# Kernel tuning notes

Measured on AMD Instinct MI355X. Metric: run time of the kernel, lower is better.

The kernel has to match this reference:

```python
import jax, jax.numpy as jnp
import numpy as np

N = 50000
E = 800000
D = 128
L = 2


def setup_inputs() -> dict:
    key = jax.random.key(0)
    ks = jax.random.split(key, 8)
    x = jax.random.normal(ks[0], (N, D), dtype=jnp.float32)
    edge_index = jax.random.randint(ks[1], (2, E), 0, N, dtype=jnp.int64)
    s = 1.0 / np.sqrt(D)
    Wl = jax.random.uniform(ks[2], (L, D, D), jnp.float32, -s, s)  # neighbor transform (with bias)
    bl = jax.random.uniform(ks[3], (L, D), jnp.float32, -s, s)
    Wr = jax.random.uniform(ks[4], (L, D, D), jnp.float32, -s, s)  # root/self transform (no bias)
    W = jax.random.uniform(ks[5], (D, D), jnp.float32, -s, s)      # final Linear
    b = jax.random.uniform(ks[6], (D,), jnp.float32, -s, s)
    return {"x": x, "edge_index": edge_index, "Wl": Wl, "bl": bl, "Wr": Wr, "W": W, "b": b}


def reference(x, edge_index, Wl, bl, Wr, W, b):
    src, dst = edge_index[0], edge_index[1]
    n = x.shape[0]
    for l in range(Wl.shape[0]):
        # gather neighbor (source) features, scatter-max into destination nodes
        agg = jax.ops.segment_max(x[src], dst, num_segments=n)  # [N, D]
        agg = jnp.where(jnp.isneginf(agg), 0.0, agg)  # PyG: isolated nodes -> 0
        # SAGEConv: lin_l(agg) + lin_r(x)
        x = agg @ Wl[l].T + bl[l] + x @ Wr[l].T
        x = jax.nn.relu(x)
    return x @ W.T + b
```

## Files before the change

kernel.cpp:

```cpp
#include <hip/hip_runtime.h>
#include <math.h>

#define NN 50000
#define NE 800000
#define DD 128
#define NBUCK 196
#define PTILE 4096
#define PBLOCKS 196
#define CONVB 6250

typedef unsigned short u16;
typedef short s8v __attribute__((ext_vector_type(8)));
typedef float f16v __attribute__((ext_vector_type(16)));

__device__ __forceinline__ u16 f2bf(float f) {
    unsigned u = __float_as_uint(f);
    return (u16)((u + 0x7FFFu + ((u >> 16) & 1u)) >> 16);
}
__device__ __forceinline__ float bflo(unsigned u) { return __uint_as_float(u << 16); }
__device__ __forceinline__ float bfhi(unsigned u) { return __uint_as_float(u & 0xFFFF0000u); }

__device__ __forceinline__ void pack_one(const float* __restrict__ Wl,
                                         const float* __restrict__ Wr,
                                         bool two, int o, u16* __restrict__ out) {
    int j = o & 7;
    int l = (o >> 3) & 63;
    int cn = o >> 9;
    int n = cn & 3;
    int c = cn >> 2;
    int colj = n * 32 + (l & 31);
    int k = c * 16 + (l >> 5) * 8 + j;
    float v;
    if (two) v = (k < DD) ? Wl[colj * DD + k] : Wr[colj * DD + (k - DD)];
    else     v = Wl[colj * DD + k];
    out[o] = f2bf(v);
}

__global__ __launch_bounds__(256) void prep_kernel(
        const float4* __restrict__ x4, ushort4* __restrict__ hb0,
        const float* __restrict__ Wl, const float* __restrict__ Wr,
        const float* __restrict__ W,
        u16* __restrict__ Bpk0, u16* __restrict__ Bpk1, u16* __restrict__ Bpkf,
        int* __restrict__ bcnt) {
    int bid = blockIdx.x;
    int tid = threadIdx.x;
    if (bid < CONVB) {
        int i = bid * 256 + tid;
        float4 v = x4[i];
        ushort4 o;
        o.x = f2bf(v.x); o.y = f2bf(v.y); o.z = f2bf(v.z); o.w = f2bf(v.w);
        hb0[i] = o;
    } else if (bid < CONVB + 128) {
        pack_one(Wl, Wr, true, (bid - CONVB) * 256 + tid, Bpk0);
    } else if (bid < CONVB + 256) {
        pack_one(Wl + DD * DD, Wr + DD * DD, true, (bid - CONVB - 128) * 256 + tid, Bpk1);
    } else if (bid < CONVB + 320) {
        pack_one(W, W, false, (bid - CONVB - 256) * 256 + tid, Bpkf);
    } else {
        if (tid < NBUCK) bcnt[tid] = 0;
    }
}

__global__ __launch_bounds__(256) void bucket_hist(const int* __restrict__ ei,
                                                   int* __restrict__ bcnt) {
    __shared__ int h[NBUCK];
    for (int i = threadIdx.x; i < NBUCK; i += 256) h[i] = 0;
    __syncthreads();
    int e0 = blockIdx.x * PTILE;
#pragma unroll
    for (int i = 0; i < 16; i++) {
        int e = e0 + i * 256 + threadIdx.x;
        if (e < NE) atomicAdd(&h[ei[NE + e] >> 8], 1);
    }
    __syncthreads();
    for (int i = threadIdx.x; i < NBUCK; i += 256)
        if (h[i]) atomicAdd(&bcnt[i], h[i]);
}

__global__ __launch_bounds__(256) void bucket_scan(const int* __restrict__ bcnt,
                                                   int* __restrict__ bbase,
                                                   int* __restrict__ bcur,
                                                   int* __restrict__ rowptr) {
    __shared__ int s[256];
    int t = threadIdx.x;
    int v = (t < NBUCK) ? bcnt[t] : 0;
    s[t] = v;
    __syncthreads();
    for (int o = 1; o < 256; o <<= 1) {
        int u = (t >= o) ? s[t - o] : 0;
        __syncthreads();
        s[t] += u;
        __syncthreads();
    }
    int ex = s[t] - v;
    if (t < NBUCK) { bbase[t] = ex; bcur[t] = ex; }
    if (t == 0) rowptr[NN] = NE;
}

__global__ __launch_bounds__(256) void bucket_partition(const int* __restrict__ ei,
                                                        int* __restrict__ bcur,
                                                        unsigned* __restrict__ packed) {
    __shared__ int h[NBUCK];
    __shared__ int base[NBUCK];
    int t = threadIdx.x;
    for (int i = t; i < NBUCK; i += 256) h[i] = 0;
    __syncthreads();
    int e0 = blockIdx.x * PTILE;
    int dsts[16], srcs[16];
#pragma unroll
    for (int i = 0; i < 16; i++) {
        int e = e0 + i * 256 + t;
        if (e < NE) {
            dsts[i] = ei[NE + e];
            srcs[i] = ei[e];
            atomicAdd(&h[dsts[i] >> 8], 1);
        } else dsts[i] = -1;
    }
    __syncthreads();
    for (int i = t; i < NBUCK; i += 256) {
        int c = h[i];
        base[i] = c ? atomicAdd(&bcur[i], c) : 0;
    }
    __syncthreads();
    for (int i = t; i < NBUCK; i += 256) h[i] = 0;
    __syncthreads();
#pragma unroll
    for (int i = 0; i < 16; i++) {
        if (dsts[i] >= 0) {
            int bk = dsts[i] >> 8;
            int r = atomicAdd(&h[bk], 1);
            packed[base[bk] + r] = (unsigned)srcs[i] | ((unsigned)(dsts[i] & 255) << 16);
        }
    }
}

__global__ __launch_bounds__(256) void bucket_csr(const unsigned* __restrict__ packed,
                                                  const int* __restrict__ bcnt,
                                                  const int* __restrict__ bbase,
                                                  int* __restrict__ rowptr,
                                                  int* __restrict__ col) {
    __shared__ int deg[256];
    __shared__ int off[256];
    int bk = blockIdx.x;
    int cnt = bcnt[bk], base = bbase[bk];
    int t = threadIdx.x;
    deg[t] = 0;
    __syncthreads();
    for (int i = t; i < cnt; i += 256) atomicAdd(&deg[packed[base + i] >> 16], 1);
    __syncthreads();
    int v = deg[t];
    off[t] = v;
    __syncthreads();
    for (int o = 1; o < 256; o <<= 1) {
        int u = (t >= o) ? off[t - o] : 0;
        __syncthreads();
        off[t] += u;
        __syncthreads();
    }
    int ex = off[t] - v;
    int node = (bk << 8) + t;
    if (node < NN) rowptr[node] = base + ex;
    deg[t] = ex;
    __syncthreads();
    for (int i = t; i < cnt; i += 256) {
        unsigned p = packed[base + i];
        int dl = p >> 16;
        int r = atomicAdd(&deg[dl], 1);
        col[base + r] = (int)(p & 0xFFFFu);
    }
}

__device__ __forceinline__ void vmax8(float* m, uint4 v) {
    m[0] = fmaxf(m[0], bflo(v.x)); m[1] = fmaxf(m[1], bfhi(v.x));
    m[2] = fmaxf(m[2], bflo(v.y)); m[3] = fmaxf(m[3], bfhi(v.y));
    m[4] = fmaxf(m[4], bflo(v.z)); m[5] = fmaxf(m[5], bfhi(v.z));
    m[6] = fmaxf(m[6], bflo(v.w)); m[7] = fmaxf(m[7], bfhi(v.w));
}

template<bool FINAL>
__global__ __launch_bounds__(256) void fused_layer(
        const u16* __restrict__ hsrc,
        const int* __restrict__ rowptr,
        const int* __restrict__ col,
        const u16* __restrict__ Bpk,
        const float* __restrict__ bias,
        const u16* __restrict__ Bpkf,
        const float* __restrict__ bfin,
        void* __restrict__ outv) {
    __shared__ u16 As[128 * 128];
    char* Ab = (char*)As;
    int tid = threadIdx.x;
    int row0 = blockIdx.x * 128;
    const uint4* xb4 = (const uint4*)hsrc;

    {
        int j = tid & 15;
        int nl0 = tid >> 4;
        for (int p = 0; p < 8; p++) {
            int rl = (p << 4) + nl0;
            int node = row0 + rl;
            uint4 o = make_uint4(0u, 0u, 0u, 0u);
            if (node < NN) {
                int s0 = rowptr[node], s1 = rowptr[node + 1];
                if (s0 < s1) {
                    float m0[8], m1[8], m2[8], m3[8];
#pragma unroll
                    for (int q = 0; q < 8; q++) { m0[q] = m1[q] = m2[q] = m3[q] = -INFINITY; }
                    int i = s0;
                    for (; i + 8 <= s1; i += 8) {
                        int c0 = col[i],     c1 = col[i + 1], c2 = col[i + 2], c3 = col[i + 3];
                        int c4 = col[i + 4], c5 = col[i + 5], c6 = col[i + 6], c7 = col[i + 7];
                        uint4 v0 = xb4[(size_t)c0 * 16 + j];
                        uint4 v1 = xb4[(size_t)c1 * 16 + j];
                        uint4 v2 = xb4[(size_t)c2 * 16 + j];
                        uint4 v3 = xb4[(size_t)c3 * 16 + j];
                        uint4 v4 = xb4[(size_t)c4 * 16 + j];
                        uint4 v5 = xb4[(size_t)c5 * 16 + j];
                        uint4 v6 = xb4[(size_t)c6 * 16 + j];
                        uint4 v7 = xb4[(size_t)c7 * 16 + j];
                        vmax8(m0, v0); vmax8(m1, v1); vmax8(m2, v2); vmax8(m3, v3);
                        vmax8(m0, v4); vmax8(m1, v5); vmax8(m2, v6); vmax8(m3, v7);
                    }
                    for (; i + 4 <= s1; i += 4) {
                        int c0 = col[i], c1 = col[i + 1], c2 = col[i + 2], c3 = col[i + 3];
                        uint4 v0 = xb4[(size_t)c0 * 16 + j];
                        uint4 v1 = xb4[(size_t)c1 * 16 + j];
                        uint4 v2 = xb4[(size_t)c2 * 16 + j];
                        uint4 v3 = xb4[(size_t)c3 * 16 + j];
                        vmax8(m0, v0); vmax8(m1, v1); vmax8(m2, v2); vmax8(m3, v3);
                    }
                    for (; i < s1; i++) {
                        uint4 v = xb4[(size_t)col[i] * 16 + j];
                        vmax8(m0, v);
                    }
#pragma unroll
                    for (int q = 0; q < 8; q++)
                        m0[q] = fmaxf(fmaxf(m0[q], m1[q]), fmaxf(m2[q], m3[q]));
                    o.x = (__float_as_uint(m0[0]) >> 16) | (__float_as_uint(m0[1]) & 0xFFFF0000u);
                    o.y = (__float_as_uint(m0[2]) >> 16) | (__float_as_uint(m0[3]) & 0xFFFF0000u);
                    o.z = (__float_as_uint(m0[4]) >> 16) | (__float_as_uint(m0[5]) & 0xFFFF0000u);
                    o.w = (__float_as_uint(m0[6]) >> 16) | (__float_as_uint(m0[7]) & 0xFFFF0000u);
                }
            }
            *(uint4*)(Ab + rl * 256 + ((j << 4) ^ ((rl & 7) << 4))) = o;
        }
    }
    __syncthreads();

    int wt = tid >> 6;
    int lane = tid & 63;
    int arl = wt * 32 + (lane & 31);
    int rg = row0 + arl;
    if (rg > NN - 1) rg = NN - 1;
    int koff = (lane >> 5) * 8;
    int swz = (arl & 7) << 4;
    const s8v* Bv = (const s8v*)Bpk;

    f16v acc[4];
#pragma unroll
    for (int n = 0; n < 4; n++) acc[n] = (f16v)(0.0f);

#pragma unroll
    for (int c = 0; c < 16; c++) {
        s8v a;
        if (c < 8)
            a = *(const s8v*)(Ab + arl * 256 + (((c * 16 + koff) * 2) ^ swz));
        else
            a = *(const s8v*)(hsrc + (size_t)rg * DD + (c - 8) * 16 + koff);
#pragma unroll
        for (int n = 0; n < 4; n++) {
            s8v b = Bv[(c * 4 + n) * 64 + lane];
            acc[n] = __builtin_amdgcn_mfma_f32_32x32x16_bf16(a, b, acc[n], 0, 0, 0);
        }
    }

    int rowadd = 4 * (lane >> 5);
    if constexpr (!FINAL) {
        u16* hdst = (u16*)outv;
#pragma unroll
        for (int n = 0; n < 4; n++) {
            int colj = n * 32 + (lane & 31);
            float bj = bias[colj];
#pragma unroll
            for (int r = 0; r < 16; r++) {
                int row = row0 + wt * 32 + (r & 3) + 8 * (r >> 2) + rowadd;
                if (row < NN)
                    hdst[(size_t)row * DD + colj] = f2bf(fmaxf(acc[n][r] + bj, 0.0f));
            }
        }
    } else {
        __syncthreads();
#pragma unroll
        for (int n = 0; n < 4; n++) {
            int colj = n * 32 + (lane & 31);
            float bj = bias[colj];
#pragma unroll
            for (int r = 0; r < 16; r++) {
                int rloc = wt * 32 + (r & 3) + 8 * (r >> 2) + rowadd;
                float v = fmaxf(acc[n][r] + bj, 0.0f);
                *(u16*)(Ab + rloc * 256 + ((colj * 2) ^ ((rloc & 7) << 4))) = f2bf(v);
            }
        }
        __syncthreads();
        const s8v* Bvf = (const s8v*)Bpkf;
        f16v acc2[4];
#pragma unroll
        for (int n = 0; n < 4; n++) acc2[n] = (f16v)(0.0f);
#pragma unroll
        for (int c = 0; c < 8; c++) {
            s8v a = *(const s8v*)(Ab + arl * 256 + (((c * 16 + koff) * 2) ^ swz));
#pragma unroll
            for (int n = 0; n < 4; n++) {
                s8v b = Bvf[(c * 4 + n) * 64 + lane];
                acc2[n] = __builtin_amdgcn_mfma_f32_32x32x16_bf16(a, b, acc2[n], 0, 0, 0);
            }
        }
        float* fout = (float*)outv;
#pragma unroll
        for (int n = 0; n < 4; n++) {
            int colj = n * 32 + (lane & 31);
            float bj = bfin[colj];
#pragma unroll
            for (int r = 0; r < 16; r++) {
                int row = row0 + wt * 32 + (r & 3) + 8 * (r >> 2) + rowadd;
                if (row < NN)
                    fout[(size_t)row * DD + colj] = acc2[n][r] + bj;
            }
        }
    }
}

extern "C" void kernel_launch(void* const* d_in, const int* in_sizes, int n_in,
                              void* d_out, int out_size, void* d_ws, size_t ws_size,
                              hipStream_t stream) {
    const float* x  = (const float*)d_in[0];
    const int*   ei = (const int*)d_in[1];
    const float* Wl = (const float*)d_in[2];
    const float* bl = (const float*)d_in[3];
    const float* Wr = (const float*)d_in[4];
    const float* W  = (const float*)d_in[5];
    const float* b  = (const float*)d_in[6];
    float* out = (float*)d_out;

    u16* aggb = (u16*)d_ws;
    u16* hb0  = aggb + (size_t)NN * DD;
    u16* hb1  = hb0 + (size_t)NN * DD;
    u16* Bpk0 = hb1 + (size_t)NN * DD;
    u16* Bpk1 = Bpk0 + 32768;
    u16* Bpkf = Bpk1 + 32768;
    unsigned* packed = (unsigned*)(Bpkf + 16384);
    int* col    = (int*)(packed + NE);
    int* rowptr = col + NE;
    int* bcnt   = rowptr + NN + 1;
    int* bbase  = bcnt + NBUCK;
    int* bcur   = bbase + NBUCK;

    dim3 blk(256);
    int gemmBlocks = (NN + 127) / 128;
    int prepBlocks = CONVB + 320 + 1;

    prep_kernel<<<prepBlocks, blk, 0, stream>>>(
        (const float4*)x, (ushort4*)hb0, Wl, Wr, W, Bpk0, Bpk1, Bpkf, bcnt);

    bucket_hist<<<PBLOCKS, blk, 0, stream>>>(ei, bcnt);
    bucket_scan<<<1, blk, 0, stream>>>(bcnt, bbase, bcur, rowptr);
    bucket_partition<<<PBLOCKS, blk, 0, stream>>>(ei, bcur, packed);
    bucket_csr<<<NBUCK, blk, 0, stream>>>(packed, bcnt, bbase, rowptr, col);

    fused_layer<false><<<gemmBlocks, blk, 0, stream>>>(
        hb0, rowptr, col, Bpk0, bl, nullptr, nullptr, hb1);

    fused_layer<true><<<gemmBlocks, blk, 0, stream>>>(
        hb1, rowptr, col, Bpk1, bl + DD, Bpkf, b, out);
}
```

Measured before the change: 247.8 us.

## Split fused aggregate+GEMM into separate kernels and fold CSR build steps

```diff
diff --git a/kernel.cpp b/kernel.cpp
--- a/kernel.cpp
+++ b/kernel.cpp
@@ -5,8 +5,8 @@
 #define NE 800000
 #define DD 128
 #define NBUCK 196
-#define PTILE 4096
-#define PBLOCKS 196
+#define EPB 2048
+#define PB 391
 #define CONVB 6250
 
 typedef unsigned short u16;
@@ -19,6 +19,11 @@
 }
 __device__ __forceinline__ float bflo(unsigned u) { return __uint_as_float(u << 16); }
 __device__ __forceinline__ float bfhi(unsigned u) { return __uint_as_float(u & 0xFFFF0000u); }
+
+__global__ __launch_bounds__(256) void zero_kernel(int* __restrict__ p, int n) {
+    int i = threadIdx.x + blockIdx.x * 256;
+    if (i < n) p[i] = 0;
+}
 
 __device__ __forceinline__ void pack_one(const float* __restrict__ Wl,
                                          const float* __restrict__ Wr,
@@ -41,7 +46,7 @@
         const float* __restrict__ Wl, const float* __restrict__ Wr,
         const float* __restrict__ W,
         u16* __restrict__ Bpk0, u16* __restrict__ Bpk1, u16* __restrict__ Bpkf,
-        int* __restrict__ bcnt) {
+        const int* __restrict__ ei, int* __restrict__ bcnt) {
     int bid = blockIdx.x;
     int tid = threadIdx.x;
     if (bid < CONVB) {
@@ -57,58 +62,48 @@
     } else if (bid < CONVB + 320) {
         pack_one(W, W, false, (bid - CONVB - 256) * 256 + tid, Bpkf);
     } else {
-        if (tid < NBUCK) bcnt[tid] = 0;
-    }
-}
-
-__global__ __launch_bounds__(256) void bucket_hist(const int* __restrict__ ei,
-                                                   int* __restrict__ bcnt) {
-    __shared__ int h[NBUCK];
-    for (int i = threadIdx.x; i < NBUCK; i += 256) h[i] = 0;
-    __syncthreads();
-    int e0 = blockIdx.x * PTILE;
-#pragma unroll
-    for (int i = 0; i < 16; i++) {
-        int e = e0 + i * 256 + threadIdx.x;
-        if (e < NE) atomicAdd(&h[ei[NE + e] >> 8], 1);
-    }
-    __syncthreads();
-    for (int i = threadIdx.x; i < NBUCK; i += 256)
-        if (h[i]) atomicAdd(&bcnt[i], h[i]);
-}
-
-__global__ __launch_bounds__(256) void bucket_scan(const int* __restrict__ bcnt,
-                                                   int* __restrict__ bbase,
-                                                   int* __restrict__ bcur,
-                                                   int* __restrict__ rowptr) {
-    __shared__ int s[256];
-    int t = threadIdx.x;
-    int v = (t < NBUCK) ? bcnt[t] : 0;
-    s[t] = v;
-    __syncthreads();
-    for (int o = 1; o < 256; o <<= 1) {
-        int u = (t >= o) ? s[t - o] : 0;
-        __syncthreads();
-        s[t] += u;
-        __syncthreads();
-    }
-    int ex = s[t] - v;
-    if (t < NBUCK) { bbase[t] = ex; bcur[t] = ex; }
-    if (t == 0) rowptr[NN] = NE;
+        __shared__ int h[NBUCK];
+        for (int i = tid; i < NBUCK; i += 256) h[i] = 0;
+        __syncthreads();
+        int e0 = (bid - (CONVB + 320)) * EPB;
+#pragma unroll
+        for (int i = 0; i < 8; i++) {
+            int e = e0 + i * 256 + tid;
+            if (e < NE) atomicAdd(&h[ei[NE + e] >> 8], 1);
+        }
+        __syncthreads();
+        for (int i = tid; i < NBUCK; i += 256)
+            if (h[i]) atomicAdd(&bcnt[i], h[i]);
+    }
 }
 
 __global__ __launch_bounds__(256) void bucket_partition(const int* __restrict__ ei,
-                                                        int* __restrict__ bcur,
-                                                        unsigned* __restrict__ packed) {
+                                                        const int* __restrict__ bcnt,
+                                                        int* __restrict__ claim,
+                                                        unsigned* __restrict__ packed,
+                                                        int* __restrict__ rowptr) {
+    __shared__ int sc[256];
+    __shared__ int bb[NBUCK];
     __shared__ int h[NBUCK];
     __shared__ int base[NBUCK];
     int t = threadIdx.x;
+    int v = (t < NBUCK) ? bcnt[t] : 0;
+    sc[t] = v;
+    __syncthreads();
+    for (int o = 1; o < 256; o <<= 1) {
+        int u = (t >= o) ? sc[t - o] : 0;
+        __syncthreads();
+        sc[t] += u;
+        __syncthreads();
+    }
+    if (t < NBUCK) bb[t] = sc[t] - v;
+    if (t == 0 && blockIdx.x == 0) rowptr[NN] = NE;
     for (int i = t; i < NBUCK; i += 256) h[i] = 0;
     __syncthreads();
-    int e0 = blockIdx.x * PTILE;
-    int dsts[16], srcs[16];
-#pragma unroll
-    for (int i = 0; i < 16; i++) {
+    int e0 = blockIdx.x * EPB;
+    int dsts[8], srcs[8];
+#pragma unroll
+    for (int i = 0; i < 8; i++) {
         int e = e0 + i * 256 + t;
         if (e < NE) {
             dsts[i] = ei[NE + e];
@@ -119,13 +114,13 @@
     __syncthreads();
     for (int i = t; i < NBUCK; i += 256) {
         int c = h[i];
-        base[i] = c ? atomicAdd(&bcur[i], c) : 0;
+        base[i] = c ? bb[i] + atomicAdd(&claim[i], c) : 0;
     }
     __syncthreads();
     for (int i = t; i < NBUCK; i += 256) h[i] = 0;
     __syncthreads();
 #pragma unroll
-    for (int i = 0; i < 16; i++) {
+    for (int i = 0; i < 8; i++) {
         if (dsts[i] >= 0) {
             int bk = dsts[i] >> 8;
             int r = atomicAdd(&h[bk], 1);
@@ -136,14 +131,24 @@
 
 __global__ __launch_bounds__(256) void bucket_csr(const unsigned* __restrict__ packed,
                                                   const int* __restrict__ bcnt,
-                                                  const int* __restrict__ bbase,
                                                   int* __restrict__ rowptr,
                                                   int* __restrict__ col) {
+    __shared__ int sc[256];
     __shared__ int deg[256];
     __shared__ int off[256];
+    int t = threadIdx.x;
+    int v0 = (t < NBUCK) ? bcnt[t] : 0;
+    sc[t] = v0;
+    __syncthreads();
+    for (int o = 1; o < 256; o <<= 1) {
+        int u = (t >= o) ? sc[t - o] : 0;
+        __syncthreads();
+        sc[t] += u;
+        __syncthreads();
+    }
     int bk = blockIdx.x;
-    int cnt = bcnt[bk], base = bbase[bk];
-    int t = threadIdx.x;
+    int cnt = bcnt[bk];
+    int base = sc[bk] - cnt;
     deg[t] = 0;
     __syncthreads();
     for (int i = t; i < cnt; i += 256) atomicAdd(&deg[packed[base + i] >> 16], 1);
@@ -177,78 +182,116 @@
     m[6] = fmaxf(m[6], bflo(v.w)); m[7] = fmaxf(m[7], bfhi(v.w));
 }
 
-template<bool FINAL>
-__global__ __launch_bounds__(256) void fused_layer(
-        const u16* __restrict__ hsrc,
-        const int* __restrict__ rowptr,
-        const int* __restrict__ col,
-        const u16* __restrict__ Bpk,
-        const float* __restrict__ bias,
-        const u16* __restrict__ Bpkf,
-        const float* __restrict__ bfin,
-        void* __restrict__ outv) {
+__global__ __launch_bounds__(256) void agg_kernel_bf(const uint4* __restrict__ xb4,
+                                                     const int* __restrict__ row_ptr,
+                                                     const int* __restrict__ col,
+                                                     uint4* __restrict__ aggb4) {
+    int node = blockIdx.x * 16 + (threadIdx.x >> 4);
+    if (node >= NN) return;
+    int j = threadIdx.x & 15;
+    int s0 = row_ptr[node], s1 = row_ptr[node + 1];
+    if (s0 == s1) {
+        aggb4[(size_t)node * 16 + j] = make_uint4(0, 0, 0, 0);
+        return;
+    }
+    float m0[8], m1[8], m2[8], m3[8];
+#pragma unroll
+    for (int q = 0; q < 8; q++) { m0[q] = m1[q] = m2[q] = m3[q] = -INFINITY; }
+    int i = s0;
+    for (; i + 8 <= s1; i += 8) {
+        int c0 = col[i],     c1 = col[i + 1], c2 = col[i + 2], c3 = col[i + 3];
+        int c4 = col[i + 4], c5 = col[i + 5], c6 = col[i + 6], c7 = col[i + 7];
+        uint4 v0 = xb4[(size_t)c0 * 16 + j];
+        uint4 v1 = xb4[(size_t)c1 * 16 + j];
+        uint4 v2 = xb4[(size_t)c2 * 16 + j];
+        uint4 v3 = xb4[(size_t)c3 * 16 + j];
+        uint4 v4 = xb4[(size_t)c4 * 16 + j];
+        uint4 v5 = xb4[(size_t)c5 * 16 + j];
+        uint4 v6 = xb4[(size_t)c6 * 16 + j];
+        uint4 v7 = xb4[(size_t)c7 * 16 + j];
+        vmax8(m0, v0); vmax8(m1, v1); vmax8(m2, v2); vmax8(m3, v3);
+        vmax8(m0, v4); vmax8(m1, v5); vmax8(m2, v6); vmax8(m3, v7);
+    }
+    for (; i + 4 <= s1; i += 4) {
+        int c0 = col[i], c1 = col[i + 1], c2 = col[i + 2], c3 = col[i + 3];
+        uint4 v0 = xb4[(size_t)c0 * 16 + j];
+        uint4 v1 = xb4[(size_t)c1 * 16 + j];
+        uint4 v2 = xb4[(size_t)c2 * 16 + j];
+        uint4 v3 = xb4[(size_t)c3 * 16 + j];
+        vmax8(m0, v0); vmax8(m1, v1); vmax8(m2, v2); vmax8(m3, v3);
+    }
+    for (; i < s1; i++) {
+        uint4 v = xb4[(size_t)col[i] * 16 + j];
+        vmax8(m0, v);
+    }
+#pragma unroll
+    for (int q = 0; q < 8; q++) m0[q] = fmaxf(fmaxf(m0[q], m1[q]), fmaxf(m2[q], m3[q]));
+    uint4 o;
+    o.x = (__float_as_uint(m0[0]) >> 16) | (__float_as_uint(m0[1]) & 0xFFFF0000u);
+    o.y = (__float_as_uint(m0[2]) >> 16) | (__float_as_uint(m0[3]) & 0xFFFF0000u);
+    o.z = (__float_as_uint(m0[4]) >> 16) | (__float_as_uint(m0[5]) & 0xFFFF0000u);
+    o.w = (__float_as_uint(m0[6]) >> 16) | (__float_as_uint(m0[7]) & 0xFFFF0000u);
+    aggb4[(size_t)node * 16 + j] = o;
+}
+
+__global__ __launch_bounds__(256) void mfma_gemm0(const u16* __restrict__ srcA,
+                                                  const u16* __restrict__ srcB,
+                                                  const u16* __restrict__ Bpk,
+                                                  const float* __restrict__ bias,
+                                                  u16* __restrict__ outh) {
+    int tid = threadIdx.x;
+    int wt = tid >> 6;
+    int lane = tid & 63;
+    int row0 = blockIdx.x * 128 + wt * 32;
+    int rload = row0 + (lane & 31);
+    if (rload > NN - 1) rload = NN - 1;
+    int koff = (lane >> 5) * 8;
+    const s8v* Bv = (const s8v*)Bpk;
+
+    f16v acc[4];
+#pragma unroll
+    for (int n = 0; n < 4; n++) acc[n] = (f16v)(0.0f);
+
+#pragma unroll
+    for (int c = 0; c < 16; c++) {
+        const u16* s = srcA;
+        int kk = c * 16;
+        if (c >= 8) { s = srcB; kk = (c - 8) * 16; }
+        s8v a = *(const s8v*)(s + (size_t)rload * DD + kk + koff);
+#pragma unroll
+        for (int n = 0; n < 4; n++) {
+            s8v b = Bv[(c * 4 + n) * 64 + lane];
+            acc[n] = __builtin_amdgcn_mfma_f32_32x32x16_bf16(a, b, acc[n], 0, 0, 0);
+        }
+    }
+
+    int rowadd = 4 * (lane >> 5);
+#pragma unroll
+    for (int n = 0; n < 4; n++) {
+        int colj = n * 32 + (lane & 31);
+        float bj = bias[colj];
+#pragma unroll
+        for (int r = 0; r < 16; r++) {
+            int row = row0 + (r & 3) + 8 * (r >> 2) + rowadd;
+            if (row < NN)
+                outh[(size_t)row * DD + colj] = f2bf(fmaxf(acc[n][r] + bj, 0.0f));
+        }
+    }
+}
+
+__global__ __launch_bounds__(256) void gemm_final(const u16* __restrict__ srcA,
+                                                  const u16* __restrict__ srcB,
+                                                  const u16* __restrict__ Bpk,
+                                                  const float* __restrict__ bias,
+                                                  const u16* __restrict__ Bpkf,
+                                                  const float* __restrict__ bfin,
+                                                  float* __restrict__ out) {
     __shared__ u16 As[128 * 128];
     char* Ab = (char*)As;
     int tid = threadIdx.x;
-    int row0 = blockIdx.x * 128;
-    const uint4* xb4 = (const uint4*)hsrc;
-
-    {
-        int j = tid & 15;
-        int nl0 = tid >> 4;
-        for (int p = 0; p < 8; p++) {
-            int rl = (p << 4) + nl0;
-            int node = row0 + rl;
-            uint4 o = make_uint4(0u, 0u, 0u, 0u);
-            if (node < NN) {
-                int s0 = rowptr[node], s1 = rowptr[node + 1];
-                if (s0 < s1) {
-                    float m0[8], m1[8], m2[8], m3[8];
-#pragma unroll
-                    for (int q = 0; q < 8; q++) { m0[q] = m1[q] = m2[q] = m3[q] = -INFINITY; }
-                    int i = s0;
-                    for (; i + 8 <= s1; i += 8) {
-                        int c0 = col[i],     c1 = col[i + 1], c2 = col[i + 2], c3 = col[i + 3];
-                        int c4 = col[i + 4], c5 = col[i + 5], c6 = col[i + 6], c7 = col[i + 7];
-                        uint4 v0 = xb4[(size_t)c0 * 16 + j];
-                        uint4 v1 = xb4[(size_t)c1 * 16 + j];
-                        uint4 v2 = xb4[(size_t)c2 * 16 + j];
-                        uint4 v3 = xb4[(size_t)c3 * 16 + j];
-                        uint4 v4 = xb4[(size_t)c4 * 16 + j];
-                        uint4 v5 = xb4[(size_t)c5 * 16 + j];
-                        uint4 v6 = xb4[(size_t)c6 * 16 + j];
-                        uint4 v7 = xb4[(size_t)c7 * 16 + j];
-                        vmax8(m0, v0); vmax8(m1, v1); vmax8(m2, v2); vmax8(m3, v3);
-                        vmax8(m0, v4); vmax8(m1, v5); vmax8(m2, v6); vmax8(m3, v7);
-                    }
-                    for (; i + 4 <= s1; i += 4) {
-                        int c0 = col[i], c1 = col[i + 1], c2 = col[i + 2], c3 = col[i + 3];
-                        uint4 v0 = xb4[(size_t)c0 * 16 + j];
-                        uint4 v1 = xb4[(size_t)c1 * 16 + j];
-                        uint4 v2 = xb4[(size_t)c2 * 16 + j];
-                        uint4 v3 = xb4[(size_t)c3 * 16 + j];
-                        vmax8(m0, v0); vmax8(m1, v1); vmax8(m2, v2); vmax8(m3, v3);
-                    }
-                    for (; i < s1; i++) {
-                        uint4 v = xb4[(size_t)col[i] * 16 + j];
-                        vmax8(m0, v);
-                    }
-#pragma unroll
-                    for (int q = 0; q < 8; q++)
-                        m0[q] = fmaxf(fmaxf(m0[q], m1[q]), fmaxf(m2[q], m3[q]));
-                    o.x = (__float_as_uint(m0[0]) >> 16) | (__float_as_uint(m0[1]) & 0xFFFF0000u);
-                    o.y = (__float_as_uint(m0[2]) >> 16) | (__float_as_uint(m0[3]) & 0xFFFF0000u);
-                    o.z = (__float_as_uint(m0[4]) >> 16) | (__float_as_uint(m0[5]) & 0xFFFF0000u);
-                    o.w = (__float_as_uint(m0[6]) >> 16) | (__float_as_uint(m0[7]) & 0xFFFF0000u);
-                }
-            }
-            *(uint4*)(Ab + rl * 256 + ((j << 4) ^ ((rl & 7) << 4))) = o;
-        }
-    }
-    __syncthreads();
-
     int wt = tid >> 6;
     int lane = tid & 63;
+    int row0 = blockIdx.x * 128;
     int arl = wt * 32 + (lane & 31);
     int rg = row0 + arl;
     if (rg > NN - 1) rg = NN - 1;
@@ -262,11 +305,10 @@
 
 #pragma unroll
     for (int c = 0; c < 16; c++) {
-        s8v a;
-        if (c < 8)
-            a = *(const s8v*)(Ab + arl * 256 + (((c * 16 + koff) * 2) ^ swz));
-        else
-            a = *(const s8v*)(hsrc + (size_t)rg * DD + (c - 8) * 16 + koff);
+        const u16* s = srcA;
+        int kk = c * 16;
+        if (c >= 8) { s = srcB; kk = (c - 8) * 16; }
+        s8v a = *(const s8v*)(s + (size_t)rg * DD + kk + koff);
 #pragma unroll
         for (int n = 0; n < 4; n++) {
             s8v b = Bv[(c * 4 + n) * 64 + lane];
@@ -275,57 +317,41 @@
     }
 
     int rowadd = 4 * (lane >> 5);
-    if constexpr (!FINAL) {
-        u16* hdst = (u16*)outv;
+#pragma unroll
+    for (int n = 0; n < 4; n++) {
+        int colj = n * 32 + (lane & 31);
+        float bj = bias[colj];
+#pragma unroll
+        for (int r = 0; r < 16; r++) {
+            int rloc = wt * 32 + (r & 3) + 8 * (r >> 2) + rowadd;
+            float v = fmaxf(acc[n][r] + bj, 0.0f);
+            *(u16*)(Ab + rloc * 256 + ((colj * 2) ^ ((rloc & 7) << 4))) = f2bf(v);
+        }
+    }
+    __syncthreads();
+
+    const s8v* Bvf = (const s8v*)Bpkf;
+    f16v acc2[4];
+#pragma unroll
+    for (int n = 0; n < 4; n++) acc2[n] = (f16v)(0.0f);
+#pragma unroll
+    for (int c = 0; c < 8; c++) {
+        s8v a = *(const s8v*)(Ab + arl * 256 + (((c * 16 + koff) * 2) ^ swz));
 #pragma unroll
         for (int n = 0; n < 4; n++) {
-            int colj = n * 32 + (lane & 31);
-            float bj = bias[colj];
-#pragma unroll
-            for (int r = 0; r < 16; r++) {
-                int row = row0 + wt * 32 + (r & 3) + 8 * (r >> 2) + rowadd;
-                if (row < NN)
-                    hdst[(size_t)row * DD + colj] = f2bf(fmaxf(acc[n][r] + bj, 0.0f));
-            }
-        }
-    } else {
-        __syncthreads();
-#pragma unroll
-        for (int n = 0; n < 4; n++) {
-            int colj = n * 32 + (lane & 31);
-            float bj = bias[colj];
-#pragma unroll
-            for (int r = 0; r < 16; r++) {
-                int rloc = wt * 32 + (r & 3) + 8 * (r >> 2) + rowadd;
-                float v = fmaxf(acc[n][r] + bj, 0.0f);
-                *(u16*)(Ab + rloc * 256 + ((colj * 2) ^ ((rloc & 7) << 4))) = f2bf(v);
-            }
-        }
-        __syncthreads();
-        const s8v* Bvf = (const s8v*)Bpkf;
-        f16v acc2[4];
-#pragma unroll
-        for (int n = 0; n < 4; n++) acc2[n] = (f16v)(0.0f);
-#pragma unroll
-        for (int c = 0; c < 8; c++) {
-            s8v a = *(const s8v*)(Ab + arl * 256 + (((c * 16 + koff) * 2) ^ swz));
-#pragma unroll
-            for (int n = 0; n < 4; n++) {
-                s8v b = Bvf[(c * 4 + n) * 64 + lane];
-                acc2[n] = __builtin_amdgcn_mfma_f32_32x32x16_bf16(a, b, acc2[n], 0, 0, 0);
-            }
-        }
-        float* fout = (float*)outv;
-#pragma unroll
-        for (int n = 0; n < 4; n++) {
-            int colj = n * 32 + (lane & 31);
-            float bj = bfin[colj];
-#pragma unroll
-            for (int r = 0; r < 16; r++) {
-                int row = row0 + wt * 32 + (r & 3) + 8 * (r >> 2) + rowadd;
-                if (row < NN)
-                    fout[(size_t)row * DD + colj] = acc2[n][r] + bj;
-            }
+            s8v b = Bvf[(c * 4 + n) * 64 + lane];
+            acc2[n] = __builtin_amdgcn_mfma_f32_32x32x16_bf16(a, b, acc2[n], 0, 0, 0);
+        }
+    }
+#pragma unroll
+    for (int n = 0; n < 4; n++) {
+        int colj = n * 32 + (lane & 31);
+        float bj = bfin[colj];
+#pragma unroll
+        for (int r = 0; r < 16; r++) {
+            int row = row0 + wt * 32 + (r & 3) + 8 * (r >> 2) + rowadd;
+            if (row < NN)
+                out[(size_t)row * DD + colj] = acc2[n][r] + bj;
         }
     }
 }
@@ -352,24 +378,23 @@
     int* col    = (int*)(packed + NE);
     int* rowptr = col + NE;
     int* bcnt   = rowptr + NN + 1;
-    int* bbase  = bcnt + NBUCK;
-    int* bcur   = bbase + NBUCK;
+    int* claim  = bcnt + NBUCK;
 
     dim3 blk(256);
     int gemmBlocks = (NN + 127) / 128;
-    int prepBlocks = CONVB + 320 + 1;
-
+    int aggBlocks  = (NN + 15) / 16;
+    int prepBlocks = CONVB + 320 + PB;
+
+    zero_kernel<<<2, blk, 0, stream>>>(bcnt, 2 * NBUCK);
     prep_kernel<<<prepBlocks, blk, 0, stream>>>(
-        (const float4*)x, (ushort4*)hb0, Wl, Wr, W, Bpk0, Bpk1, Bpkf, bcnt);
-
-    bucket_hist<<<PBLOCKS, blk, 0, stream>>>(ei, bcnt);
-    bucket_scan<<<1, blk, 0, stream>>>(bcnt, bbase, bcur, rowptr);
-    bucket_partition<<<PBLOCKS, blk, 0, stream>>>(ei, bcur, packed);
-    bucket_csr<<<NBUCK, blk, 0, stream>>>(packed, bcnt, bbase, rowptr, col);
-
-    fused_layer<false><<<gemmBlocks, blk, 0, stream>>>(
-        hb0, rowptr, col, Bpk0, bl, nullptr, nullptr, hb1);
-
-    fused_layer<true><<<gemmBlocks, blk, 0, stream>>>(
-        hb1, rowptr, col, Bpk1, bl + DD, Bpkf, b, out);
-}
+        (const float4*)x, (ushort4*)hb0, Wl, Wr, W, Bpk0, Bpk1, Bpkf, ei, bcnt);
+
+    bucket_partition<<<PB, blk, 0, stream>>>(ei, bcnt, claim, packed, rowptr);
+    bucket_csr<<<NBUCK, blk, 0, stream>>>(packed, bcnt, rowptr, col);
+
+    agg_kernel_bf<<<aggBlocks, blk, 0, stream>>>((const uint4*)hb0, rowptr, col, (uint4*)aggb);
+    mfma_gemm0<<<gemmBlocks, blk, 0, stream>>>(aggb, hb0, Bpk0, bl, hb1);
+
+    agg_kernel_bf<<<aggBlocks, blk, 0, stream>>>((const uint4*)hb1, rowptr, col, (uint4*)aggb);
+    gemm_final<<<gemmBlocks, blk, 0, stream>>>(aggb, hb1, Bpk1, bl + DD, Bpkf, b, out);
+}
```

Result: faster. 235.8 us (-4.9%).
